# Kernel optimization log

Hardware: AMD Instinct MI355X
Metric: run time of the kernel (lower is better)

Reference implementation:

```python
import jax, jax.numpy as jnp
import numpy as np

B, N, E = 1, 100000, 3200000
CIN, COUT = 128, 128


def setup_inputs() -> dict:
    key = jax.random.key(0)
    k1, k2, k3, k4 = jax.random.split(key, 4)
    X = jax.random.normal(k1, (B, N, CIN), dtype=jnp.float32)
    edge_index = jax.random.randint(k2, (2, E), 0, N, dtype=jnp.int32)
    edge_weight = jax.random.uniform(k3, (E,), dtype=jnp.float32)
    # GCNConv parameters (glorot weight, zero bias)
    W = jax.random.normal(k4, (CIN, COUT), dtype=jnp.float32) * np.float32(1.0 / np.sqrt(CIN))
    b = jnp.zeros((COUT,), dtype=jnp.float32)
    return {"X": X, "edge_index": edge_index, "edge_weight": edge_weight, "W": W, "b": b}


def reference(X, edge_index, edge_weight, W, b):
    """PyG GCNConv (node_dim=1): symmetric-normalized gather -> linear -> scatter-add.
    out = D^{-1/2} (A + I) D^{-1/2} X W + b, batched over dim 0.
    """
    B_, N_, _ = X.shape
    # add self-loops with weight 1 (PyG GCNConv default fill_value=1)
    loop = jnp.arange(N_, dtype=edge_index.dtype)
    ei = jnp.concatenate([edge_index, jnp.stack([loop, loop])], axis=1)  # (2, E+N)
    ew = jnp.concatenate([edge_weight, jnp.ones((N_,), X.dtype)])        # (E+N,)
    src, dst = ei[0], ei[1]
    deg = jax.ops.segment_sum(ew, dst, num_segments=N_)                  # (N,)
    dis = jnp.where(deg > 0, jax.lax.rsqrt(deg), jnp.zeros_like(deg))
    norm = dis[src] * ew * dis[dst]                                      # (E+N,)
    h = jnp.einsum('bnc,cd->bnd', X, W)                                  # (B,N,COUT)
    msg = h[:, src] * norm[None, :, None]                                # (B,E+N,COUT) gather
    out = jnp.zeros((B_, N_, h.shape[-1]), h.dtype).at[:, dst].add(msg)  # scatter-add
    return out + b
```

## Files before the change

kernel.cpp:

```cpp
#include <hip/hip_runtime.h>

#define CIN 128
#define COUT 128
#define NB_MAX 512
#define BCAP 10240
#define EPB 8192

typedef float f32x4 __attribute__((ext_vector_type(4)));
typedef short bf16x8 __attribute__((ext_vector_type(8)));

__device__ __forceinline__ unsigned short f2bf(float x) {
    unsigned int b = __float_as_uint(x);
    b += 0x7FFFu + ((b >> 16) & 1u);
    return (unsigned short)(b >> 16);
}
__device__ __forceinline__ float bf2f_hi(unsigned int u) {
    return __uint_as_float(u & 0xFFFF0000u);
}
__device__ __forceinline__ float bf2f_lo(unsigned int u) {
    return __uint_as_float(u << 16);
}

__global__ void k_prep(const float* __restrict__ W, unsigned short* __restrict__ WB,
                       int* __restrict__ cursor, int NB, int NBz) {
    int b = blockIdx.x;
    int t = threadIdx.x;
    if (b < NBz) {
        int i = b * 256 + t;
        if (i < NB) cursor[i] = 0;
    } else {
        int pos = (b - NBz) * 2048 + t * 8;
        int lane = (pos >> 3) & 63;
        int ks   = (pos >> 9) & 3;
        int ct   = pos >> 11;
        int k = ks * 32 + (lane >> 4) * 8;
        int c = ct * 16 + (lane & 15);
        #pragma unroll
        for (int j = 0; j < 8; ++j)
            WB[pos + j] = f2bf(W[(k + j) * COUT + c]);
    }
}

__global__ __launch_bounds__(1024) void k_part(const int* __restrict__ ei, const float* __restrict__ ew,
                                               int* __restrict__ cursor,
                                               unsigned long long* __restrict__ brec,
                                               int E, int NB) {
    __shared__ int hist[NB_MAX];
    __shared__ int base_[NB_MAX];
    int t = threadIdx.x;
    int chunk0 = blockIdx.x * EPB;
    bool vec_ok = ((E & 3) == 0);

    for (int i = t; i < NB; i += 1024) hist[i] = 0;
    __syncthreads();

    #pragma unroll
    for (int k = 0; k < EPB / 4096; ++k) {
        int e0 = chunk0 + (k * 1024 + t) * 4;
        if (vec_ok && e0 + 3 < E) {
            int4 d4 = *(const int4*)(ei + E + e0);
            atomicAdd(&hist[d4.x >> 8], 1);
            atomicAdd(&hist[d4.y >> 8], 1);
            atomicAdd(&hist[d4.z >> 8], 1);
            atomicAdd(&hist[d4.w >> 8], 1);
        } else {
            for (int q = 0; q < 4; ++q) {
                int e = e0 + q;
                if (e < E) atomicAdd(&hist[ei[E + e] >> 8], 1);
            }
        }
    }
    __syncthreads();

    for (int i = t; i < NB; i += 1024) {
        int c = hist[i];
        base_[i] = (c > 0) ? atomicAdd(&cursor[i], c) : 0;
        hist[i] = 0;
    }
    __syncthreads();

#define PLACE(ss, dd, ww) do {                                                    \
        int b_ = (dd) >> 8;                                                       \
        unsigned int q_ = (unsigned int)((ww) * 32767.0f + 0.5f);                 \
        int lp_ = atomicAdd(&hist[b_], 1);                                        \
        int pos_ = base_[b_] + lp_;                                               \
        if (pos_ < BCAP)                                                          \
            brec[(size_t)b_ * BCAP + pos_] =                                      \
                ((unsigned long long)((dd) & 255) << 32) |                        \
                (((unsigned int)(ss) << 15) | q_);                                \
    } while (0)

    #pragma unroll
    for (int k = 0; k < EPB / 4096; ++k) {
        int e0 = chunk0 + (k * 1024 + t) * 4;
        if (vec_ok && e0 + 3 < E) {
            int4 s4 = *(const int4*)(ei + e0);
            int4 d4 = *(const int4*)(ei + E + e0);
            float4 w4 = *(const float4*)(ew + e0);
            PLACE(s4.x, d4.x, w4.x);
            PLACE(s4.y, d4.y, w4.y);
            PLACE(s4.z, d4.z, w4.z);
            PLACE(s4.w, d4.w, w4.w);
        } else {
            for (int q = 0; q < 4; ++q) {
                int e = e0 + q;
                if (e < E) PLACE(ei[e], ei[E + e], ew[e]);
            }
        }
    }
#undef PLACE
}

__global__ __launch_bounds__(256) void k_sortdeg(const unsigned long long* __restrict__ brec,
                                                 const int* __restrict__ cursor,
                                                 unsigned int* __restrict__ srec,
                                                 int2* __restrict__ rowinfo,
                                                 float* __restrict__ dis, int N) {
    __shared__ int histA[256];
    __shared__ int scanB[256];
    __shared__ int degq[256];
    __shared__ unsigned int stage[BCAP];
    int t = threadIdx.x;
    int b = blockIdx.x;
    int cnt = min(cursor[b], BCAP);
    const unsigned long long* r = brec + (size_t)b * BCAP;

    histA[t] = 0; degq[t] = 0;
    __syncthreads();

    for (int j = t; j < cnt; j += 256) {
        unsigned long long v = r[j];
        int dl = (int)(v >> 32);
        atomicAdd(&histA[dl], 1);
        atomicAdd(&degq[dl], (int)((unsigned int)v & 0x7FFFu));
    }
    __syncthreads();

    int c = histA[t];
    scanB[t] = c;
    __syncthreads();
    #pragma unroll
    for (int off = 1; off < 256; off <<= 1) {
        int v = (t >= off) ? scanB[t - off] : 0;
        __syncthreads();
        scanB[t] += v;
        __syncthreads();
    }
    int excl = scanB[t] - c;

    int n = b * 256 + t;
    if (n < N) {
        dis[n] = rsqrtf(1.0f + (float)degq[t] * (1.0f / 32767.0f));
        rowinfo[n] = make_int2(b * BCAP + excl, c);
    }
    histA[t] = excl;
    __syncthreads();

    for (int j = t; j < cnt; j += 256) {
        unsigned long long v = r[j];
        int dl = (int)(v >> 32);
        int pos = atomicAdd(&histA[dl], 1);
        stage[pos] = (unsigned int)v;
    }
    __syncthreads();

    unsigned int* so = srec + (size_t)b * BCAP;
    for (int j = t; j < cnt; j += 256) so[j] = stage[j];
}

__global__ __launch_bounds__(256) void k_gemm(const float* __restrict__ X,
                                              const unsigned short* __restrict__ WB,
                                              const float* __restrict__ dis,
                                              unsigned short* __restrict__ h, int N) {
    __shared__ unsigned short WBs[8 * 4 * 64 * 8];
    __shared__ unsigned short outs[4][16 * 128];
    int t = threadIdx.x;
    int w = t >> 6, l = t & 63;
    int n0 = blockIdx.x * 64;

    {
        const uint4* src = (const uint4*)WB;
        uint4* dst = (uint4*)WBs;
        #pragma unroll
        for (int i = 0; i < 8; ++i) dst[t + i * 256] = src[t + i * 256];
    }

    int rowg = n0 + w * 16 + (l & 15);
    int rcl = min(rowg, N - 1);
    int kbase = (l >> 4) * 8;
    bf16x8 afrag[4];
    #pragma unroll
    for (int ks = 0; ks < 4; ++ks) {
        const float* xp = X + (size_t)rcl * CIN + ks * 32 + kbase;
        float4 x0 = *(const float4*)xp;
        float4 x1 = *(const float4*)(xp + 4);
        bf16x8 a;
        a[0] = (short)f2bf(x0.x); a[1] = (short)f2bf(x0.y);
        a[2] = (short)f2bf(x0.z); a[3] = (short)f2bf(x0.w);
        a[4] = (short)f2bf(x1.x); a[5] = (short)f2bf(x1.y);
        a[6] = (short)f2bf(x1.z); a[7] = (short)f2bf(x1.w);
        afrag[ks] = a;
    }

    __syncthreads();

    f32x4 acc[8];
    #pragma unroll
    for (int ct = 0; ct < 8; ++ct) acc[ct] = (f32x4){0.f, 0.f, 0.f, 0.f};

    const bf16x8* wb = (const bf16x8*)WBs;
    #pragma unroll
    for (int ct = 0; ct < 8; ++ct) {
        #pragma unroll
        for (int ks = 0; ks < 4; ++ks) {
            bf16x8 b = wb[(ct * 4 + ks) * 64 + l];
            acc[ct] = __builtin_amdgcn_mfma_f32_16x16x32_bf16(afrag[ks], b, acc[ct], 0, 0, 0);
        }
    }

    int rb = n0 + w * 16 + (l >> 4) * 4;
    float4 d4 = *(const float4*)(dis + rb);
    unsigned short* ow = &outs[w][0];
    #pragma unroll
    for (int ct = 0; ct < 8; ++ct) {
        int ocol = ct * 16 + (l & 15);
        int orow = (l >> 4) * 4;
        ow[(orow + 0) * 128 + ocol] = f2bf(acc[ct][0] * d4.x);
        ow[(orow + 1) * 128 + ocol] = f2bf(acc[ct][1] * d4.y);
        ow[(orow + 2) * 128 + ocol] = f2bf(acc[ct][2] * d4.z);
        ow[(orow + 3) * 128 + ocol] = f2bf(acc[ct][3] * d4.w);
    }

    size_t plane1 = (size_t)N * 64;
    #pragma unroll
    for (int i = 0; i < 4; ++i) {
        int off = i * 1024 + l * 16;
        int orow = off >> 8;
        int col = (off & 255) >> 1;
        int node = n0 + w * 16 + orow;
        if (node < N) {
            uint4 v = *(const uint4*)((const char*)ow + off);
            unsigned short* dst = h + (col < 64 ? 0 : plane1) + (size_t)node * 64 + (col & 63);
            *(uint4*)dst = v;
        }
    }
}

__global__ __launch_bounds__(256) void k_agg(const unsigned short* __restrict__ h,
                                             const unsigned int* __restrict__ srec,
                                             const int2* __restrict__ rowinfo,
                                             const float* __restrict__ dis,
                                             const float* __restrict__ bias,
                                             float* __restrict__ out, int N, int plane) {
    int wave = threadIdx.x >> 6;
    int lane = threadIdx.x & 63;
    int grp  = lane >> 5;
    int l32  = lane & 31;
    int slot = l32 >> 3;
    int cl   = l32 & 7;
    int node = blockIdx.x * 8 + wave * 2 + grp;
    bool valid = node < N;
    int2 ri = valid ? rowinfo[node] : make_int2(0, 0);
    const unsigned int* r = srec + ri.x;
    int m = ri.y;
    const uint4* hu = (const uint4*)(h + (size_t)plane * N * 64);

    float a[8] = {0.f, 0.f, 0.f, 0.f, 0.f, 0.f, 0.f, 0.f};
    if (valid && slot == 0) {
        uint4 us = hu[(size_t)node * 8 + cl];
        a[0] = bf2f_lo(us.x); a[1] = bf2f_hi(us.x);
        a[2] = bf2f_lo(us.y); a[3] = bf2f_hi(us.y);
        a[4] = bf2f_lo(us.z); a[5] = bf2f_hi(us.z);
        a[6] = bf2f_lo(us.w); a[7] = bf2f_hi(us.w);
    }

#define LOAD_REC(dst, base_j) do {                                           \
        _Pragma("unroll")                                                    \
        for (int u = 0; u < 2; ++u) {                                        \
            int j_ = (base_j) + u * 4 + slot;                                \
            dst[u] = (j_ < m) ? __builtin_nontemporal_load(r + j_) : 0u;     \
        } } while (0)

    unsigned int rrc[2];
    LOAD_REC(rrc, 0);
    for (int jb = 0; jb < m; jb += 8) {
        unsigned int rrn[2];
        LOAD_REC(rrn, jb + 8);
        uint4 v0 = hu[(size_t)(rrc[0] >> 15) * 8 + cl];
        uint4 v1 = hu[(size_t)(rrc[1] >> 15) * 8 + cl];
        float w0 = (float)(rrc[0] & 0x7FFFu) * (1.0f / 32767.0f);
        float w1 = (float)(rrc[1] & 0x7FFFu) * (1.0f / 32767.0f);
        a[0] += w0 * bf2f_lo(v0.x); a[1] += w0 * bf2f_hi(v0.x);
        a[2] += w0 * bf2f_lo(v0.y); a[3] += w0 * bf2f_hi(v0.y);
        a[4] += w0 * bf2f_lo(v0.z); a[5] += w0 * bf2f_hi(v0.z);
        a[6] += w0 * bf2f_lo(v0.w); a[7] += w0 * bf2f_hi(v0.w);
        a[0] += w1 * bf2f_lo(v1.x); a[1] += w1 * bf2f_hi(v1.x);
        a[2] += w1 * bf2f_lo(v1.y); a[3] += w1 * bf2f_hi(v1.y);
        a[4] += w1 * bf2f_lo(v1.z); a[5] += w1 * bf2f_hi(v1.z);
        a[6] += w1 * bf2f_lo(v1.w); a[7] += w1 * bf2f_hi(v1.w);
        rrc[0] = rrn[0]; rrc[1] = rrn[1];
    }
#undef LOAD_REC

    #pragma unroll
    for (int i = 0; i < 8; ++i) {
        a[i] += __shfl_xor(a[i], 8);
        a[i] += __shfl_xor(a[i], 16);
    }

    if (valid && slot == 0) {
        float dn = dis[node];
        int c0 = plane * 64 + cl * 8;
        float4 b0 = *(const float4*)(bias + c0);
        float4 b1 = *(const float4*)(bias + c0 + 4);
        f32x4 o0 = {a[0] * dn + b0.x, a[1] * dn + b0.y, a[2] * dn + b0.z, a[3] * dn + b0.w};
        f32x4 o1 = {a[4] * dn + b1.x, a[5] * dn + b1.y, a[6] * dn + b1.z, a[7] * dn + b1.w};
        f32x4* op = (f32x4*)(out + (size_t)node * COUT + c0);
        __builtin_nontemporal_store(o0, op);
        __builtin_nontemporal_store(o1, op + 1);
    }
}

extern "C" void kernel_launch(void* const* d_in, const int* in_sizes, int n_in,
                              void* d_out, int out_size, void* d_ws, size_t ws_size,
                              hipStream_t stream) {
    const float* X    = (const float*)d_in[0];
    const int*   ei   = (const int*)d_in[1];
    const float* ew   = (const float*)d_in[2];
    const float* W    = (const float*)d_in[3];
    const float* bias = (const float*)d_in[4];
    float* out = (float*)d_out;

    int E = in_sizes[2];
    int N = out_size / COUT;
    int NB = (N + 255) >> 8;
    int NBz = (NB + 255) >> 8;

    char* ws = (char*)d_ws;
    unsigned short*     h    = (unsigned short*)ws;     ws += (size_t)N * COUT * 2;
    unsigned long long* brec = (unsigned long long*)ws; ws += (size_t)NB * BCAP * 8;
    unsigned int*       srec = (unsigned int*)ws;       ws += (size_t)NB * BCAP * 4;
    int2*               rinf = (int2*)ws;               ws += (size_t)N * 8;
    float*              dis  = (float*)ws;              ws += (size_t)(N + 64) * 4;
    int*                cur  = (int*)ws;                ws += (size_t)NB * 4;
    unsigned short*     WB   = (unsigned short*)ws;     ws += 8 * 4 * 64 * 8 * 2;

    k_prep   <<<NBz + 8, 256, 0, stream>>>(W, WB, cur, NB, NBz);
    k_part   <<<(E + EPB - 1) / EPB, 1024, 0, stream>>>(ei, ew, cur, brec, E, NB);
    k_sortdeg<<<NB, 256, 0, stream>>>(brec, cur, srec, rinf, dis, N);
    k_gemm   <<<(N + 63) / 64, 256, 0, stream>>>(X, WB, dis, h, N);
    k_agg    <<<(N + 7) / 8, 256, 0, stream>>>(h, srec, rinf, dis, bias, out, N, 0);
    k_agg    <<<(N + 7) / 8, 256, 0, stream>>>(h, srec, rinf, dis, bias, out, N, 1);
}
```

Baseline: 191.5 us.

## Pipeline neighbor gathers through LDS with global_load_lds and multi-stage prefetch

Rewrites the aggregation inner loop so neighbor feature rows are gathered asynchronously into per-wave LDS ring buffers with global_load_lds, AGG_D stages deep. Edge records are prefetched further ahead and manual s_waitcnt plus sched_barrier control the overlap. The goal is to keep more gather loads in flight and hide memory latency. In exchange it adds LDS use, hand-counted vmcnt values that depend on exact instruction counts, and wave-uniform loop bounds (max of the two node groups) that run extra masked iterations.

```diff
diff --git a/kernel.cpp b/kernel.cpp
--- a/kernel.cpp
+++ b/kernel.cpp
@@ -5,6 +5,7 @@
 #define NB_MAX 512
 #define BCAP 10240
 #define EPB 8192
+#define AGG_D 4
 
 typedef float f32x4 __attribute__((ext_vector_type(4)));
 typedef short bf16x8 __attribute__((ext_vector_type(8)));
@@ -252,55 +253,98 @@
                                              const float* __restrict__ dis,
                                              const float* __restrict__ bias,
                                              float* __restrict__ out, int N, int plane) {
-    int wave = threadIdx.x >> 6;
-    int lane = threadIdx.x & 63;
+    __shared__ char gbuf[4][AGG_D][2048];
+    int t = threadIdx.x;
+    int wv   = t >> 6;
+    int lane = t & 63;
     int grp  = lane >> 5;
     int l32  = lane & 31;
     int slot = l32 >> 3;
     int cl   = l32 & 7;
-    int node = blockIdx.x * 8 + wave * 2 + grp;
+    int node = blockIdx.x * 8 + wv * 2 + grp;
     bool valid = node < N;
-    int2 ri = valid ? rowinfo[node] : make_int2(0, 0);
+    int nodec = valid ? node : (N - 1);
+    int2 ri = rowinfo[nodec];
     const unsigned int* r = srec + ri.x;
-    int m = ri.y;
+    int m = valid ? ri.y : 0;
+    int mw = max(m, __shfl_xor(m, 32));
     const uint4* hu = (const uint4*)(h + (size_t)plane * N * 64);
+    char* mybuf = &gbuf[wv][0][0];
+
+#define SB0() __builtin_amdgcn_sched_barrier(0)
+#define LRS(d0, d1, basej) do {                                              \
+        int j0_ = (basej) + slot;                                            \
+        int j1_ = (basej) + 4 + slot;                                        \
+        unsigned int q0_ = __builtin_nontemporal_load(r + j0_);              \
+        unsigned int q1_ = __builtin_nontemporal_load(r + j1_);              \
+        d0 = (j0_ < m) ? q0_ : 0u;                                           \
+        d1 = (j1_ < m) ? q1_ : 0u;                                           \
+    } while (0)
+#define ISS(dbuf, r0v, r1v) do {                                                         \
+        const uint4* g0_ = hu + (size_t)((r0v) >> 15) * 8 + cl;                          \
+        const uint4* g1_ = hu + (size_t)((r1v) >> 15) * 8 + cl;                          \
+        __builtin_amdgcn_global_load_lds(                                                \
+            (__attribute__((address_space(1))) const void*)g0_,                         \
+            (__attribute__((address_space(3))) void*)(dbuf), 16, 0, 0);                 \
+        __builtin_amdgcn_global_load_lds(                                                \
+            (__attribute__((address_space(1))) const void*)g1_,                         \
+            (__attribute__((address_space(3))) void*)((dbuf) + 1024), 16, 0, 0);        \
+    } while (0)
+#define ACC2(r0v, r1v, v0, v1) do {                                                     \
+        float w0_ = (float)((r0v) & 0x7FFFu) * (1.0f / 32767.0f);                       \
+        float w1_ = (float)((r1v) & 0x7FFFu) * (1.0f / 32767.0f);                       \
+        a[0] += w0_ * bf2f_lo(v0.x); a[1] += w0_ * bf2f_hi(v0.x);                       \
+        a[2] += w0_ * bf2f_lo(v0.y); a[3] += w0_ * bf2f_hi(v0.y);                       \
+        a[4] += w0_ * bf2f_lo(v0.z); a[5] += w0_ * bf2f_hi(v0.z);                       \
+        a[6] += w0_ * bf2f_lo(v0.w); a[7] += w0_ * bf2f_hi(v0.w);                       \
+        a[0] += w1_ * bf2f_lo(v1.x); a[1] += w1_ * bf2f_hi(v1.x);                       \
+        a[2] += w1_ * bf2f_lo(v1.y); a[3] += w1_ * bf2f_hi(v1.y);                       \
+        a[4] += w1_ * bf2f_lo(v1.z); a[5] += w1_ * bf2f_hi(v1.z);                       \
+        a[6] += w1_ * bf2f_lo(v1.w); a[7] += w1_ * bf2f_hi(v1.w);                       \
+    } while (0)
 
     float a[8] = {0.f, 0.f, 0.f, 0.f, 0.f, 0.f, 0.f, 0.f};
-    if (valid && slot == 0) {
-        uint4 us = hu[(size_t)node * 8 + cl];
-        a[0] = bf2f_lo(us.x); a[1] = bf2f_hi(us.x);
-        a[2] = bf2f_lo(us.y); a[3] = bf2f_hi(us.y);
-        a[4] = bf2f_lo(us.z); a[5] = bf2f_hi(us.z);
-        a[6] = bf2f_lo(us.w); a[7] = bf2f_hi(us.w);
-    }
-
-#define LOAD_REC(dst, base_j) do {                                           \
-        _Pragma("unroll")                                                    \
-        for (int u = 0; u < 2; ++u) {                                        \
-            int j_ = (base_j) + u * 4 + slot;                                \
-            dst[u] = (j_ < m) ? __builtin_nontemporal_load(r + j_) : 0u;     \
-        } } while (0)
-
-    unsigned int rrc[2];
-    LOAD_REC(rrc, 0);
-    for (int jb = 0; jb < m; jb += 8) {
-        unsigned int rrn[2];
-        LOAD_REC(rrn, jb + 8);
-        uint4 v0 = hu[(size_t)(rrc[0] >> 15) * 8 + cl];
-        uint4 v1 = hu[(size_t)(rrc[1] >> 15) * 8 + cl];
-        float w0 = (float)(rrc[0] & 0x7FFFu) * (1.0f / 32767.0f);
-        float w1 = (float)(rrc[1] & 0x7FFFu) * (1.0f / 32767.0f);
-        a[0] += w0 * bf2f_lo(v0.x); a[1] += w0 * bf2f_hi(v0.x);
-        a[2] += w0 * bf2f_lo(v0.y); a[3] += w0 * bf2f_hi(v0.y);
-        a[4] += w0 * bf2f_lo(v0.z); a[5] += w0 * bf2f_hi(v0.z);
-        a[6] += w0 * bf2f_lo(v0.w); a[7] += w0 * bf2f_hi(v0.w);
-        a[0] += w1 * bf2f_lo(v1.x); a[1] += w1 * bf2f_hi(v1.x);
-        a[2] += w1 * bf2f_lo(v1.y); a[3] += w1 * bf2f_hi(v1.y);
-        a[4] += w1 * bf2f_lo(v1.z); a[5] += w1 * bf2f_hi(v1.z);
-        a[6] += w1 * bf2f_lo(v1.w); a[7] += w1 * bf2f_hi(v1.w);
-        rrc[0] = rrn[0]; rrc[1] = rrn[1];
-    }
-#undef LOAD_REC
+    if (slot == 0) {
+        uint4 us = hu[(size_t)nodec * 8 + cl];
+        if (valid) {
+            a[0] = bf2f_lo(us.x); a[1] = bf2f_hi(us.x);
+            a[2] = bf2f_lo(us.y); a[3] = bf2f_hi(us.y);
+            a[4] = bf2f_lo(us.z); a[5] = bf2f_hi(us.z);
+            a[6] = bf2f_lo(us.w); a[7] = bf2f_hi(us.w);
+        }
+    }
+    SB0();
+
+    unsigned int rA0, rA1, rB0, rB1, rC0, rC1, rD0, rD1, rE0, rE1;
+    LRS(rA0, rA1, 0);  SB0(); ISS(mybuf + 0 * 2048, rA0, rA1); SB0();
+    LRS(rB0, rB1, 8);  SB0(); ISS(mybuf + 1 * 2048, rB0, rB1); SB0();
+    LRS(rC0, rC1, 16); SB0(); ISS(mybuf + 2 * 2048, rC0, rC1); SB0();
+    LRS(rD0, rD1, 24); SB0(); ISS(mybuf + 3 * 2048, rD0, rD1); SB0();
+    LRS(rE0, rE1, 32); SB0();
+
+    for (int jb = 0; jb < mw; jb += 8) {
+        char* slotbuf = mybuf + ((jb >> 3) & (AGG_D - 1)) * 2048;
+        asm volatile("s_waitcnt vmcnt(12)" ::: "memory");
+        SB0();
+        uint4 v0 = *(const uint4*)(slotbuf + lane * 16);
+        uint4 v1 = *(const uint4*)(slotbuf + 1024 + lane * 16);
+        asm volatile("s_waitcnt lgkmcnt(0)" ::: "memory");
+        SB0();
+        ACC2(rA0, rA1, v0, v1);
+        SB0();
+        ISS(slotbuf, rE0, rE1);
+        SB0();
+        unsigned int t0, t1;
+        LRS(t0, t1, jb + 40);
+        SB0();
+        rA0 = rB0; rA1 = rB1; rB0 = rC0; rB1 = rC1;
+        rC0 = rD0; rC1 = rD1; rD0 = rE0; rD1 = rE1;
+        rE0 = t0;  rE1 = t1;
+    }
+#undef SB0
+#undef LRS
+#undef ISS
+#undef ACC2
 
     #pragma unroll
     for (int i = 0; i < 8; ++i) {
```

Result: slower. 272.8 us (median of 4 runs) (+42.5%).

## Merge two-plane aggregation into single pass over full-width bf16 rows

Applied to the files above, without the earlier changes.

The GEMM now writes h as contiguous 128-column bf16 rows instead of two 64-column planes. The aggregation kernel runs once instead of twice, with 16 lanes covering a full 256-byte row and two edge slots per node instead of four. This halves the passes over the edge records and the launches, but each gather becomes wider and the whole h array must stay in cache at once rather than one half at a time. The GEMM also gains a stray nontemporal load whose result is discarded, which may add a redundant read of X.

```diff
diff --git a/kernel.cpp b/kernel.cpp
--- a/kernel.cpp
+++ b/kernel.cpp
@@ -192,13 +192,16 @@
     #pragma unroll
     for (int ks = 0; ks < 4; ++ks) {
         const float* xp = X + (size_t)rcl * CIN + ks * 32 + kbase;
-        float4 x0 = *(const float4*)xp;
-        float4 x1 = *(const float4*)(xp + 4);
+        float4 x0 = __builtin_nontemporal_load((const f32x4*)xp)
+                        [0] == 0.f ? *(const float4*)xp : *(const float4*)xp;
+        (void)x0;
+        float4 xa = *(const float4*)xp;
+        float4 xb = *(const float4*)(xp + 4);
         bf16x8 a;
-        a[0] = (short)f2bf(x0.x); a[1] = (short)f2bf(x0.y);
-        a[2] = (short)f2bf(x0.z); a[3] = (short)f2bf(x0.w);
-        a[4] = (short)f2bf(x1.x); a[5] = (short)f2bf(x1.y);
-        a[6] = (short)f2bf(x1.z); a[7] = (short)f2bf(x1.w);
+        a[0] = (short)f2bf(xa.x); a[1] = (short)f2bf(xa.y);
+        a[2] = (short)f2bf(xa.z); a[3] = (short)f2bf(xa.w);
+        a[4] = (short)f2bf(xb.x); a[5] = (short)f2bf(xb.y);
+        a[6] = (short)f2bf(xb.z); a[7] = (short)f2bf(xb.w);
         afrag[ks] = a;
     }
 
@@ -231,7 +234,6 @@
         ow[(orow + 3) * 128 + ocol] = f2bf(acc[ct][3] * d4.w);
     }
 
-    size_t plane1 = (size_t)N * 64;
     #pragma unroll
     for (int i = 0; i < 4; ++i) {
         int off = i * 1024 + l * 16;
@@ -240,8 +242,7 @@
         int node = n0 + w * 16 + orow;
         if (node < N) {
             uint4 v = *(const uint4*)((const char*)ow + off);
-            unsigned short* dst = h + (col < 64 ? 0 : plane1) + (size_t)node * 64 + (col & 63);
-            *(uint4*)dst = v;
+            *(uint4*)(h + (size_t)node * COUT + col) = v;
         }
     }
 }
@@ -251,23 +252,22 @@
                                              const int2* __restrict__ rowinfo,
                                              const float* __restrict__ dis,
                                              const float* __restrict__ bias,
-                                             float* __restrict__ out, int N, int plane) {
+                                             float* __restrict__ out, int N) {
     int wave = threadIdx.x >> 6;
     int lane = threadIdx.x & 63;
-    int grp  = lane >> 5;
-    int l32  = lane & 31;
-    int slot = l32 >> 3;
-    int cl   = l32 & 7;
-    int node = blockIdx.x * 8 + wave * 2 + grp;
+    int slot = lane >> 4;
+    int sl   = slot & 1;
+    int cl   = lane & 15;
+    int node = blockIdx.x * 8 + wave * 2 + (slot >> 1);
     bool valid = node < N;
     int2 ri = valid ? rowinfo[node] : make_int2(0, 0);
     const unsigned int* r = srec + ri.x;
     int m = ri.y;
-    const uint4* hu = (const uint4*)(h + (size_t)plane * N * 64);
+    const uint4* hu = (const uint4*)h;
 
     float a[8] = {0.f, 0.f, 0.f, 0.f, 0.f, 0.f, 0.f, 0.f};
-    if (valid && slot == 0) {
-        uint4 us = hu[(size_t)node * 8 + cl];
+    if (valid && sl == 0) {
+        uint4 us = hu[(size_t)node * 16 + cl];
         a[0] = bf2f_lo(us.x); a[1] = bf2f_hi(us.x);
         a[2] = bf2f_lo(us.y); a[3] = bf2f_hi(us.y);
         a[4] = bf2f_lo(us.z); a[5] = bf2f_hi(us.z);
@@ -276,41 +276,39 @@
 
 #define LOAD_REC(dst, base_j) do {                                           \
         _Pragma("unroll")                                                    \
-        for (int u = 0; u < 2; ++u) {                                        \
-            int j_ = (base_j) + u * 4 + slot;                                \
-            dst[u] = (j_ < m) ? __builtin_nontemporal_load(r + j_) : 0u;     \
+        for (int u = 0; u < 4; ++u) {                                        \
+            int j_ = (base_j) + u * 2 + sl;                                  \
+            unsigned int q_ = 0u;                                            \
+            if (j_ < m) q_ = __builtin_nontemporal_load(r + j_);             \
+            dst[u] = q_;                                                     \
         } } while (0)
 
-    unsigned int rrc[2];
+    unsigned int rrc[4];
     LOAD_REC(rrc, 0);
-    for (int jb = 0; jb < m; jb += 8) {
-        unsigned int rrn[2];
-        LOAD_REC(rrn, jb + 8);
-        uint4 v0 = hu[(size_t)(rrc[0] >> 15) * 8 + cl];
-        uint4 v1 = hu[(size_t)(rrc[1] >> 15) * 8 + cl];
-        float w0 = (float)(rrc[0] & 0x7FFFu) * (1.0f / 32767.0f);
-        float w1 = (float)(rrc[1] & 0x7FFFu) * (1.0f / 32767.0f);
-        a[0] += w0 * bf2f_lo(v0.x); a[1] += w0 * bf2f_hi(v0.x);
-        a[2] += w0 * bf2f_lo(v0.y); a[3] += w0 * bf2f_hi(v0.y);
-        a[4] += w0 * bf2f_lo(v0.z); a[5] += w0 * bf2f_hi(v0.z);
-        a[6] += w0 * bf2f_lo(v0.w); a[7] += w0 * bf2f_hi(v0.w);
-        a[0] += w1 * bf2f_lo(v1.x); a[1] += w1 * bf2f_hi(v1.x);
-        a[2] += w1 * bf2f_lo(v1.y); a[3] += w1 * bf2f_hi(v1.y);
-        a[4] += w1 * bf2f_lo(v1.z); a[5] += w1 * bf2f_hi(v1.z);
-        a[6] += w1 * bf2f_lo(v1.w); a[7] += w1 * bf2f_hi(v1.w);
-        rrc[0] = rrn[0]; rrc[1] = rrn[1];
+    for (int j0 = 0; j0 < m; j0 += 8) {
+        unsigned int rrn[4];
+        LOAD_REC(rrn, j0 + 8);
+        #pragma unroll
+        for (int u = 0; u < 4; ++u) {
+            unsigned int rr = rrc[u];
+            float w = (float)(rr & 0x7FFFu) * (1.0f / 32767.0f);
+            uint4 v = hu[(size_t)(rr >> 15) * 16 + cl];
+            a[0] += w * bf2f_lo(v.x); a[1] += w * bf2f_hi(v.x);
+            a[2] += w * bf2f_lo(v.y); a[3] += w * bf2f_hi(v.y);
+            a[4] += w * bf2f_lo(v.z); a[5] += w * bf2f_hi(v.z);
+            a[6] += w * bf2f_lo(v.w); a[7] += w * bf2f_hi(v.w);
+        }
+        #pragma unroll
+        for (int u = 0; u < 4; ++u) rrc[u] = rrn[u];
     }
 #undef LOAD_REC
 
     #pragma unroll
-    for (int i = 0; i < 8; ++i) {
-        a[i] += __shfl_xor(a[i], 8);
-        a[i] += __shfl_xor(a[i], 16);
-    }
-
-    if (valid && slot == 0) {
+    for (int i = 0; i < 8; ++i) a[i] += __shfl_xor(a[i], 16);
+
+    if (valid && sl == 0) {
         float dn = dis[node];
-        int c0 = plane * 64 + cl * 8;
+        int c0 = cl * 8;
         float4 b0 = *(const float4*)(bias + c0);
         float4 b1 = *(const float4*)(bias + c0 + 4);
         f32x4 o0 = {a[0] * dn + b0.x, a[1] * dn + b0.y, a[2] * dn + b0.z, a[3] * dn + b0.w};
@@ -349,6 +347,5 @@
     k_part   <<<(E + EPB - 1) / EPB, 1024, 0, stream>>>(ei, ew, cur, brec, E, NB);
     k_sortdeg<<<NB, 256, 0, stream>>>(brec, cur, srec, rinf, dis, N);
     k_gemm   <<<(N + 63) / 64, 256, 0, stream>>>(X, WB, dis, h, N);
-    k_agg    <<<(N + 7) / 8, 256, 0, stream>>>(h, srec, rinf, dis, bias, out, N, 0);
-    k_agg    <<<(N + 7) / 8, 256, 0, stream>>>(h, srec, rinf, dis, bias, out, N, 1);
-}
+    k_agg    <<<(N + 7) / 8, 256, 0, stream>>>(h, srec, rinf, dis, bias, out, N);
+}
```

Result: no change. 187.9 us (-1.9%).
